# Performance work log

Hardware: AMD Instinct MI355X
Metric: run time of the kernel (lower is better)

Reference implementation:

```python
import jax, jax.numpy as jnp
import numpy as np

D_IN = 1024
D_OUT = 1024


def setup_inputs() -> dict:
    key = jax.random.key(0)
    kx, kq, kk, kv = jax.random.split(key, 4)
    x = jax.random.normal(kx, (4, 2048, D_IN), dtype=jnp.float32)
    s = 1.0 / np.sqrt(D_IN)
    Wq = jax.random.normal(kq, (D_IN, D_OUT), dtype=jnp.float32) * s
    Wk = jax.random.normal(kk, (D_IN, D_OUT), dtype=jnp.float32) * s
    Wv = jax.random.normal(kv, (D_IN, D_OUT), dtype=jnp.float32) * s
    return {"x": x, "Wq": Wq, "Wk": Wk, "Wv": Wv}


def reference(x, Wq, Wk, Wv):
    # x: [B, S, d_in]; W*: [d_in, d_out]
    B, S, _ = x.shape
    q = x @ Wq  # [B, S, d_out]
    k = x @ Wk
    v = x @ Wv
    scale = 1.0 / jnp.sqrt(jnp.asarray(k.shape[-1], x.dtype))
    scores = jnp.einsum("bqd,bkd->bqk", q, k) * scale  # [B, S, S]
    # causal mask: positions j > i masked to -inf (triu, diagonal=1)
    causal = jnp.tril(jnp.ones((S, S), dtype=bool))
    scores = jnp.where(causal[None, :, :], scores, -jnp.inf)
    attn = jax.nn.softmax(scores, axis=-1)  # dropout p=0.0 -> identity
    return jnp.einsum("bqk,bkd->bqd", attn, v)
```

## Files before the change

kernel.cpp:

```cpp
#include <hip/hip_runtime.h>
#include <hip/hip_bf16.h>

#define NB 4
#define SB 2048
#define DD 1024
#define BM 128
#define BN 128
#define BK 32

typedef __attribute__((ext_vector_type(8))) short bf16x8;
typedef __attribute__((ext_vector_type(4))) short bf16x4;
typedef __attribute__((ext_vector_type(4))) float f32x4;
typedef unsigned int u32;

__device__ __forceinline__ float bf2f(unsigned short u) {
    return __uint_as_float(((u32)u) << 16);
}
__device__ __forceinline__ short f2bf(float f) {
    u32 u = __float_as_uint(f);
    u32 r = (u + 0x7fffu + ((u >> 16) & 1u)) >> 16;
    return (short)r;
}

__device__ __forceinline__ void wait_vm8() {
    asm volatile("s_waitcnt vmcnt(8)" ::: "memory");
}
__device__ __forceinline__ void wait_vm6() {
    asm volatile("s_waitcnt vmcnt(6)" ::: "memory");
}
__device__ __forceinline__ void wait_vm0() {
    asm volatile("s_waitcnt vmcnt(0)" ::: "memory");
}
__device__ __forceinline__ void barrier_raw() {
    __builtin_amdgcn_s_barrier();
    asm volatile("" ::: "memory");
}

__device__ __forceinline__ void mfma_step(const short* As, const short* Bs,
                                          f32x4 (&acc)[4][4], int lane, int wave)
{
    const int wm = (wave >> 1) * 64, wn = (wave & 1) * 64;
    const int fr = lane & 15;
    const int quad = lane >> 4;
    bf16x8 af[4], bf[4];
#pragma unroll
    for (int t = 0; t < 4; t++) {
        af[t] = *(const bf16x8*)&As[(wm + t * 16 + fr) * BK + quad * 8];
        bf[t] = *(const bf16x8*)&Bs[(wn + t * 16 + fr) * BK + quad * 8];
    }
#pragma unroll
    for (int mt = 0; mt < 4; mt++)
#pragma unroll
        for (int nt = 0; nt < 4; nt++)
            acc[mt][nt] = __builtin_amdgcn_mfma_f32_16x16x32_bf16(
                af[mt], bf[nt], acc[mt][nt], 0, 0, 0);
}

__device__ __forceinline__ void mfma_step_pv_swz(const short* As,
                                                 const short* Bs,
                                                 f32x4 (&acc)[2][4], int lane,
                                                 int wave)
{
    const int wm = wave * 32;
    const int fr = lane & 15;
    const int qa = (lane >> 4) ^ ((fr >> 1) & 3);
    bf16x8 af[2], bf[4];
#pragma unroll
    for (int t = 0; t < 2; t++)
        af[t] = *(const bf16x8*)&As[(wm + t * 16 + fr) * BK + qa * 8];
#pragma unroll
    for (int t = 0; t < 4; t++)
        bf[t] = *(const bf16x8*)&Bs[(t * 16 + fr) * BK + qa * 8];
#pragma unroll
    for (int mt = 0; mt < 2; mt++)
#pragma unroll
        for (int nt = 0; nt < 4; nt++)
            acc[mt][nt] = __builtin_amdgcn_mfma_f32_16x16x32_bf16(
                af[mt], bf[nt], acc[mt][nt], 0, 0, 0);
}

__device__ __forceinline__ void mfma_step256_swz(const short* As,
                                                 const short* Bs,
                                                 f32x4 (&acc)[8][4], int lane,
                                                 int wave)
{
    const int wm = (wave >> 2) * 128;
    const int wn = (wave & 3) * 64;
    const int fr = lane & 15;
    const int qa = (lane >> 4) ^ ((fr >> 1) & 3);
    bf16x8 af[8], bf[4];
#pragma unroll
    for (int t = 0; t < 8; t++)
        af[t] = *(const bf16x8*)&As[(wm + t * 16 + fr) * BK + qa * 8];
#pragma unroll
    for (int t = 0; t < 4; t++)
        bf[t] = *(const bf16x8*)&Bs[(wn + t * 16 + fr) * BK + qa * 8];
#pragma unroll
    for (int mt = 0; mt < 8; mt++)
#pragma unroll
        for (int nt = 0; nt < 4; nt++)
            acc[mt][nt] = __builtin_amdgcn_mfma_f32_16x16x32_bf16(
                af[mt], bf[nt], acc[mt][nt], 0, 0, 0);
}

__device__ __forceinline__ void stage128x32(const short* __restrict__ g, int ld,
                                            short* lds, int tid) {
    const int wave = tid >> 6, lane = tid & 63;
    const int r = lane >> 2;
    const int c = ((lane & 3) ^ ((lane >> 3) & 3)) * 8;
#pragma unroll
    for (int i = 0; i < 2; i++) {
        const int chunk = wave * 2 + i;
        const short* gp = g + (size_t)(chunk * 16 + r) * ld + c;
        __builtin_amdgcn_global_load_lds(
            (const __attribute__((address_space(1))) u32*)gp,
            (__attribute__((address_space(3))) u32*)(lds + chunk * 512 + lane * 8),
            16, 0, 0);
    }
}

__device__ __forceinline__ void stage64x32(const short* __restrict__ g, int ld,
                                           short* lds, int tid) {
    const int wave = tid >> 6, lane = tid & 63;
    const int r = lane >> 2;
    const int c = ((lane & 3) ^ ((lane >> 3) & 3)) * 8;
    const short* gp = g + (size_t)(wave * 16 + r) * ld + c;
    __builtin_amdgcn_global_load_lds(
        (const __attribute__((address_space(1))) u32*)gp,
        (__attribute__((address_space(3))) u32*)(lds + wave * 512 + lane * 8),
        16, 0, 0);
}

__device__ __forceinline__ void stage256x64(const short* __restrict__ g, int ld,
                                            short* base, int tid) {
    const int w = tid >> 6, l = tid & 63;
    const int lr = l >> 2;
    const int lc = ((l & 3) ^ ((l >> 3) & 3)) * 8;
#pragma unroll
    for (int i = 0; i < 4; i++) {
        const int ks = i >> 1;
        const int row = (i & 1) * 128 + w * 16 + lr;
        const short* gp = g + (size_t)row * ld + ks * 32 + lc;
        __builtin_amdgcn_global_load_lds(
            (const __attribute__((address_space(1))) u32*)gp,
            (__attribute__((address_space(3))) u32*)(base + i * 4096 + w * 512 + l * 8),
            16, 0, 0);
    }
}

__device__ __forceinline__ void stage_f32_128x32(const float* __restrict__ g,
                                                 int ld, short* lds, int tid) {
    const int r = tid >> 1;
    const int c = (tid & 1) * 16;
    const float* gp = &g[(size_t)r * ld + c];
    float4 v0 = *(const float4*)(gp + 0);
    float4 v1 = *(const float4*)(gp + 4);
    float4 v2 = *(const float4*)(gp + 8);
    float4 v3 = *(const float4*)(gp + 12);
    bf16x8 o0, o1;
    o0[0] = f2bf(v0.x); o0[1] = f2bf(v0.y); o0[2] = f2bf(v0.z); o0[3] = f2bf(v0.w);
    o0[4] = f2bf(v1.x); o0[5] = f2bf(v1.y); o0[6] = f2bf(v1.z); o0[7] = f2bf(v1.w);
    o1[0] = f2bf(v2.x); o1[1] = f2bf(v2.y); o1[2] = f2bf(v2.z); o1[3] = f2bf(v2.w);
    o1[4] = f2bf(v3.x); o1[5] = f2bf(v3.y); o1[6] = f2bf(v3.z); o1[7] = f2bf(v3.w);
    *(bf16x8*)&lds[r * BK + c] = o0;
    *(bf16x8*)&lds[r * BK + c + 8] = o1;
}

__global__ __launch_bounds__(256) void prep_mm(
    const float* __restrict__ x, const float* __restrict__ Wq,
    const float* __restrict__ Wk, const float* __restrict__ Wv,
    short* __restrict__ xb, short* __restrict__ Wvt, float* __restrict__ Mp4)
{
    __shared__ short As[BM * BK], Bs[BN * BK];
    __shared__ short t[64][65];
    const int bx = blockIdx.x;
    const int tid = threadIdx.x;
    if (bx < 256) {
        const int ch = bx >> 6;
        const int t64 = bx & 63;
        const int m0 = (t64 >> 3) * BM;
        const int n0 = (t64 & 7) * BN;
        const int kbase = ch * 256;
        const int lane = tid & 63, wave = tid >> 6;
        f32x4 acc[4][4];
#pragma unroll
        for (int a = 0; a < 4; a++)
#pragma unroll
            for (int b = 0; b < 4; b++) acc[a][b] = (f32x4){0.f, 0.f, 0.f, 0.f};
        for (int k0 = 0; k0 < 256; k0 += BK) {
            stage_f32_128x32(Wk + (size_t)m0 * DD + kbase + k0, DD, As, tid);
            stage_f32_128x32(Wq + (size_t)n0 * DD + kbase + k0, DD, Bs, tid);
            __syncthreads();
            mfma_step(As, Bs, acc, lane, wave);
            __syncthreads();
        }
        const int wm = (wave >> 1) * 64, wn = (wave & 1) * 64;
        const int fr = lane & 15, quad = lane >> 4;
        float* Mc = Mp4 + (size_t)ch * DD * DD;
#pragma unroll
        for (int mt = 0; mt < 4; mt++)
#pragma unroll
            for (int nt = 0; nt < 4; nt++)
#pragma unroll
                for (int r = 0; r < 4; r++) {
                    const size_t m = m0 + wm + mt * 16 + quad * 4 + r;
                    const size_t n = n0 + wn + nt * 16 + fr;
                    Mc[m * DD + n] = acc[mt][nt][r];
                }
        return;
    }
    if (bx < 4352) {
        const size_t i = ((size_t)(bx - 256) * 256 + tid) * 8;
        float4 a = *(const float4*)&x[i];
        float4 b = *(const float4*)&x[i + 4];
        bf16x8 o;
        o[0] = f2bf(a.x); o[1] = f2bf(a.y); o[2] = f2bf(a.z); o[3] = f2bf(a.w);
        o[4] = f2bf(b.x); o[5] = f2bf(b.y); o[6] = f2bf(b.z); o[7] = f2bf(b.w);
        *(bf16x8*)&xb[i] = o;
        return;
    }
    const int rr = bx - 4352;
    const int k0 = (rr & 15) * 64;
    const int n0 = (rr >> 4) * 64;
    {
        const int r = tid >> 4;
        const int c = (tid & 15) * 4;
#pragma unroll
        for (int i = 0; i < 4; i++) {
            float4 v = *(const float4*)&Wv[(size_t)(k0 + i * 16 + r) * DD + n0 + c];
            t[i * 16 + r][c + 0] = f2bf(v.x);
            t[i * 16 + r][c + 1] = f2bf(v.y);
            t[i * 16 + r][c + 2] = f2bf(v.z);
            t[i * 16 + r][c + 3] = f2bf(v.w);
        }
    }
    __syncthreads();
    {
        const int r = tid >> 3;
        const int c = (tid & 7) * 8;
#pragma unroll
        for (int i = 0; i < 2; i++) {
            bf16x8 o;
#pragma unroll
            for (int j = 0; j < 8; j++) o[j] = t[c + j][i * 32 + r];
            *(bf16x8*)&Wvt[(size_t)(n0 + i * 32 + r) * DD + k0 + c] = o;
        }
    }
}

__global__ __launch_bounds__(256) void mm_reduce(const float* __restrict__ Mp4,
                                                 short* __restrict__ Mp)
{
    const size_t e = ((size_t)blockIdx.x * 256 + threadIdx.x) * 4;
    const size_t N = (size_t)DD * DD;
    float4 s = *(const float4*)&Mp4[e];
#pragma unroll
    for (int c = 1; c < 4; c++) {
        float4 p = *(const float4*)&Mp4[c * N + e];
        s.x += p.x; s.y += p.y; s.z += p.z; s.w += p.w;
    }
    bf16x4 o;
    o[0] = f2bf(s.x); o[1] = f2bf(s.y); o[2] = f2bf(s.z); o[3] = f2bf(s.w);
    *(bf16x4*)&Mp[e] = o;
}

__global__ __launch_bounds__(512) void tv_gemm(
    const short* __restrict__ xb, const short* __restrict__ Mp,
    const short* __restrict__ Wvt, short* __restrict__ T,
    short* __restrict__ Vt)
{
    __shared__ short lds[2 * 32768];
    const int lin = blockIdx.x + 4 * blockIdx.y;
    const int swz = (lin & 7) * 16 + (lin >> 3);
    const int n0 = (swz & 3) * 256;
    const int m0 = (swz >> 2) * 256;
    const int isv = blockIdx.z;
    const short* Bt = isv ? Wvt : Mp;
    const short* Ap = xb + (size_t)m0 * DD;
    const short* Bp = Bt + (size_t)n0 * DD;
    const int tid = threadIdx.x;
    const int lane = tid & 63, wave = tid >> 6;
    f32x4 acc[8][4];
#pragma unroll
    for (int a = 0; a < 8; a++)
#pragma unroll
        for (int b = 0; b < 4; b++) acc[a][b] = (f32x4){0.f, 0.f, 0.f, 0.f};

    stage256x64(Ap, DD, lds, tid);
    stage256x64(Bp, DD, lds + 16384, tid);
    for (int j = 0; j < 16; ++j) {
        const int cur = j & 1;
        short* slot = lds + cur * 32768;
        if (j < 15) {
            short* nxt = lds + (cur ^ 1) * 32768;
            stage256x64(Ap + (j + 1) * 64, DD, nxt, tid);
            stage256x64(Bp + (j + 1) * 64, DD, nxt + 16384, tid);
            wait_vm8();
        } else {
            wait_vm0();
        }
        barrier_raw();
        __builtin_amdgcn_s_setprio(1);
        mfma_step256_swz(slot, slot + 16384, acc, lane, wave);
        mfma_step256_swz(slot + 8192, slot + 16384 + 8192, acc, lane, wave);
        __builtin_amdgcn_s_setprio(0);
        barrier_raw();
    }

    const int wm = (wave >> 2) * 128, wn = (wave & 3) * 64;
    const int fr = lane & 15, quad = lane >> 4;
    if (!isv) {
#pragma unroll
        for (int mt = 0; mt < 8; mt++)
#pragma unroll
            for (int nt = 0; nt < 4; nt++)
#pragma unroll
                for (int r = 0; r < 4; r++) {
                    const size_t m = m0 + wm + mt * 16 + quad * 4 + r;
                    const size_t n = n0 + wn + nt * 16 + fr;
                    T[m * DD + n] = f2bf(acc[mt][nt][r]);
                }
    } else {
        const int bb = m0 >> 11;
        const int s0 = (m0 & (SB - 1)) + wm + quad * 4;
        short* Vb = Vt + (size_t)bb * DD * SB;
#pragma unroll
        for (int mt = 0; mt < 8; mt++)
#pragma unroll
            for (int nt = 0; nt < 4; nt++) {
                const size_t n = n0 + wn + nt * 16 + fr;
                const size_t s = s0 + mt * 16;
                bf16x4 o;
#pragma unroll
                for (int r = 0; r < 4; r++) o[r] = f2bf(acc[mt][nt][r]);
                *(bf16x4*)&Vb[n * SB + s] = o;
            }
    }
}

__global__ __launch_bounds__(256) void scores_mfma(
    const short* __restrict__ T, const short* __restrict__ xb,
    short* __restrict__ Sc)
{
    const int bx = blockIdx.x;
    const int idx = (bx & 7) * 34 + (bx >> 3);
    int qt = (int)((__fsqrt_rn(4.f * idx + 1.f) - 1.f) * 0.5f);
    while ((qt + 1) * (qt + 2) <= idx) qt++;
    while (qt * (qt + 1) > idx) qt--;
    const int kt = idx - qt * (qt + 1);
    const int qm0 = qt * BM;
    const int kn0 = kt * 64;
    const int b = blockIdx.y;
    __shared__ short As[2 * BM * BK], Bs[2 * 64 * BK];
    const short* Tq = T + (size_t)b * SB * DD + (size_t)qm0 * DD;
    const short* Xk = xb + (size_t)b * SB * DD + (size_t)kn0 * DD;
    short* Sb = Sc + (size_t)b * SB * SB;
    const int tid = threadIdx.x;
    const int lane = tid & 63, wave = tid >> 6;
    f32x4 acc[2][4];
#pragma unroll
    for (int a = 0; a < 2; a++)
#pragma unroll
        for (int c = 0; c < 4; c++) acc[a][c] = (f32x4){0.f, 0.f, 0.f, 0.f};
    for (int k0 = 0; k0 < DD; k0 += 2 * BK) {
        stage128x32(Tq + k0, DD, As, tid);
        stage128x32(Tq + k0 + BK, DD, As + BM * BK, tid);
        stage64x32(Xk + k0, DD, Bs, tid);
        stage64x32(Xk + k0 + BK, DD, Bs + 64 * BK, tid);
        __syncthreads();
        mfma_step_pv_swz(As, Bs, acc, lane, wave);
        mfma_step_pv_swz(As + BM * BK, Bs + 64 * BK, acc, lane, wave);
        __syncthreads();
    }
    const int fr = lane & 15, quad = lane >> 4;
    const float scale = 0.03125f;
#pragma unroll
    for (int mt = 0; mt < 2; mt++)
#pragma unroll
        for (int nt = 0; nt < 4; nt++)
#pragma unroll
            for (int r = 0; r < 4; r++) {
                const size_t q = qm0 + wave * 32 + mt * 16 + quad * 4 + r;
                const size_t k = kn0 + nt * 16 + fr;
                Sb[q * SB + k] = f2bf(acc[mt][nt][r] * scale);
            }
}

__global__ __launch_bounds__(256) void softmax_kernel(short* __restrict__ Sc)
{
    const int row = blockIdx.x;
    const int i = row & (SB - 1);
    const int jlim = ((i >> 7) + 1) << 7;
    short* r = Sc + (size_t)row * SB;
    const int t = threadIdx.x;
    const int lane = t & 63, wave = t >> 6;
    __shared__ float red[8];

    const int j0 = t * 8;
    bf16x8 in = {0, 0, 0, 0, 0, 0, 0, 0};
    if (j0 <= i) in = *(const bf16x8*)&r[j0];
    float v[8];
    float mx = -1e30f;
#pragma unroll
    for (int e = 0; e < 8; e++) {
        const float s = (j0 + e <= i) ? bf2f((unsigned short)in[e]) : -1e30f;
        v[e] = s;
        mx = fmaxf(mx, s);
    }
#pragma unroll
    for (int o = 32; o > 0; o >>= 1) mx = fmaxf(mx, __shfl_down(mx, o));
    if (lane == 0) red[wave] = mx;
    __syncthreads();
    mx = fmaxf(fmaxf(red[0], red[1]), fmaxf(red[2], red[3]));

    float sum = 0.f;
#pragma unroll
    for (int e = 0; e < 8; e++) {
        const float x = (j0 + e <= i) ? __expf(v[e] - mx) : 0.f;
        v[e] = x;
        sum += x;
    }
#pragma unroll
    for (int o = 32; o > 0; o >>= 1) sum += __shfl_down(sum, o);
    if (lane == 0) red[4 + wave] = sum;
    __syncthreads();
    const float inv = 1.0f / (red[4] + red[5] + red[6] + red[7]);
    if (j0 < jlim) {
        bf16x8 o;
#pragma unroll
        for (int e = 0; e < 8; e++) o[e] = f2bf(v[e] * inv);
        *(bf16x8*)&r[j0] = o;
    }
}

__global__ __launch_bounds__(256) void pv_mfma(
    const short* __restrict__ P, const short* __restrict__ Vt,
    float* __restrict__ O)
{
    __shared__ short As[4 * BM * BK];
    __shared__ short Bs[4 * 64 * BK];
    const int n0 = blockIdx.x * 64;
    const int pair = blockIdx.y;
    const int b = blockIdx.z;
    const short* Pb = P + (size_t)b * SB * SB;
    const short* Vb = Vt + (size_t)b * DD * SB;
    float* Ob = O + (size_t)b * SB * DD;
    const int tid = threadIdx.x;
    const int lane = tid & 63, wave = tid >> 6;
    const int fr = lane & 15, quad = lane >> 4;
    for (int half = 0; half < 2; ++half) {
        const int qt = half ? (15 - pair) : pair;
        const int qm0 = qt * BM;
        const int nj = (qt + 1) * 2;
        const short* Pq = Pb + (size_t)qm0 * SB;
        const short* Vn = Vb + (size_t)n0 * SB;
        f32x4 acc[2][4];
#pragma unroll
        for (int a = 0; a < 2; a++)
#pragma unroll
            for (int c = 0; c < 4; c++) acc[a][c] = (f32x4){0.f, 0.f, 0.f, 0.f};
        stage128x32(Pq, SB, As, tid);
        stage128x32(Pq + BK, SB, As + BM * BK, tid);
        stage64x32(Vn, SB, Bs, tid);
        stage64x32(Vn + BK, SB, Bs + 64 * BK, tid);
        for (int j = 0; j < nj; ++j) {
            const int cur = j & 1;
            const short* as = As + cur * (2 * BM * BK);
            const short* bs = Bs + cur * (2 * 64 * BK);
            if (j + 1 < nj) {
                const int off = (j + 1) * 64;
                short* an = As + (cur ^ 1) * (2 * BM * BK);
                short* bn = Bs + (cur ^ 1) * (2 * 64 * BK);
                stage128x32(Pq + off, SB, an, tid);
                stage128x32(Pq + off + BK, SB, an + BM * BK, tid);
                stage64x32(Vn + off, SB, bn, tid);
                stage64x32(Vn + off + BK, SB, bn + 64 * BK, tid);
                wait_vm6();
            } else {
                wait_vm0();
            }
            barrier_raw();
            mfma_step_pv_swz(as, bs, acc, lane, wave);
            mfma_step_pv_swz(as + BM * BK, bs + 64 * BK, acc, lane, wave);
            barrier_raw();
        }
#pragma unroll
        for (int mt = 0; mt < 2; mt++)
#pragma unroll
            for (int nt = 0; nt < 4; nt++)
#pragma unroll
                for (int r = 0; r < 4; r++) {
                    const size_t q = qm0 + wave * 32 + mt * 16 + quad * 4 + r;
                    const size_t n = n0 + nt * 16 + fr;
                    Ob[q * DD + n] = acc[mt][nt][r];
                }
    }
}

extern "C" void kernel_launch(void* const* d_in, const int* in_sizes, int n_in,
                              void* d_out, int out_size, void* d_ws, size_t ws_size,
                              hipStream_t stream)
{
    const float* x  = (const float*)d_in[0];
    const float* Wq = (const float*)d_in[1];
    const float* Wk = (const float*)d_in[2];
    const float* Wv = (const float*)d_in[3];
    float* out = (float*)d_out;

    const size_t XE = (size_t)NB * SB * DD;
    const size_t WE = (size_t)DD * DD;
    short* xb  = (short*)d_ws;
    short* T   = xb + XE;
    short* Vt  = T + XE;
    short* Sc  = Vt + XE;
    float* Pp  = (float*)(Sc + (size_t)NB * SB * SB);
    short* Wvt = (short*)(Pp + (size_t)NB * 1024 * DD);
    short* Mp  = Wvt + WE;
    float* Mp4 = (float*)Sc;

    prep_mm<<<dim3(256 + 4096 + 256), 256, 0, stream>>>(
        x, Wq, Wk, Wv, xb, Wvt, Mp4);
    mm_reduce<<<dim3(1024), 256, 0, stream>>>(Mp4, Mp);
    tv_gemm<<<dim3(4, 32, 2), 512, 0, stream>>>(xb, Mp, Wvt, T, Vt);
    scores_mfma<<<dim3(272, NB), 256, 0, stream>>>(T, xb, Sc);
    softmax_kernel<<<dim3(NB * SB), 256, 0, stream>>>(Sc);
    pv_mfma<<<dim3(DD / 64, 8, NB), 256, 0, stream>>>(Sc, Vt, out);
}
```

Baseline: 222.6 us.

## Widen PV kernel tiles to 128x128 with swizzled MFMA fragment loads

The PV GEMM now computes a 128x128 output tile per block instead of 128x64, and each wave owns a 64x64 sub-tile using a new swizzled MFMA step. The grid shrinks from 512 to 256 blocks, and the wait count is adjusted for the extra V staging loads. It also raises wave priority around the MFMA section. The goal is better reuse of the staged P tile and fewer P reloads, at the cost of fewer blocks for the GPU's many CUs and more LDS and registers per block.

```diff
diff --git a/kernel.cpp b/kernel.cpp
--- a/kernel.cpp
+++ b/kernel.cpp
@@ -25,9 +25,6 @@
 __device__ __forceinline__ void wait_vm8() {
     asm volatile("s_waitcnt vmcnt(8)" ::: "memory");
 }
-__device__ __forceinline__ void wait_vm6() {
-    asm volatile("s_waitcnt vmcnt(6)" ::: "memory");
-}
 __device__ __forceinline__ void wait_vm0() {
     asm volatile("s_waitcnt vmcnt(0)" ::: "memory");
 }
@@ -47,6 +44,27 @@
     for (int t = 0; t < 4; t++) {
         af[t] = *(const bf16x8*)&As[(wm + t * 16 + fr) * BK + quad * 8];
         bf[t] = *(const bf16x8*)&Bs[(wn + t * 16 + fr) * BK + quad * 8];
+    }
+#pragma unroll
+    for (int mt = 0; mt < 4; mt++)
+#pragma unroll
+        for (int nt = 0; nt < 4; nt++)
+            acc[mt][nt] = __builtin_amdgcn_mfma_f32_16x16x32_bf16(
+                af[mt], bf[nt], acc[mt][nt], 0, 0, 0);
+}
+
+__device__ __forceinline__ void mfma_step_swz(const short* As, const short* Bs,
+                                              f32x4 (&acc)[4][4], int lane,
+                                              int wave)
+{
+    const int wm = (wave >> 1) * 64, wn = (wave & 1) * 64;
+    const int fr = lane & 15;
+    const int qa = (lane >> 4) ^ ((fr >> 1) & 3);
+    bf16x8 af[4], bf[4];
+#pragma unroll
+    for (int t = 0; t < 4; t++) {
+        af[t] = *(const bf16x8*)&As[(wm + t * 16 + fr) * BK + qa * 8];
+        bf[t] = *(const bf16x8*)&Bs[(wn + t * 16 + fr) * BK + qa * 8];
     }
 #pragma unroll
     for (int mt = 0; mt < 4; mt++)
@@ -437,10 +455,9 @@
     const short* __restrict__ P, const short* __restrict__ Vt,
     float* __restrict__ O)
 {
-    __shared__ short As[4 * BM * BK];
-    __shared__ short Bs[4 * 64 * BK];
-    const int n0 = blockIdx.x * 64;
-    const int pair = blockIdx.y;
+    __shared__ short As[2 * 8192], Bs[2 * 8192];
+    const int pair = blockIdx.x;
+    const int n0 = blockIdx.y * 128;
     const int b = blockIdx.z;
     const short* Pb = P + (size_t)b * SB * SB;
     const short* Vb = Vt + (size_t)b * DD * SB;
@@ -454,44 +471,47 @@
         const int nj = (qt + 1) * 2;
         const short* Pq = Pb + (size_t)qm0 * SB;
         const short* Vn = Vb + (size_t)n0 * SB;
-        f32x4 acc[2][4];
-#pragma unroll
-        for (int a = 0; a < 2; a++)
+        f32x4 acc[4][4];
+#pragma unroll
+        for (int a = 0; a < 4; a++)
 #pragma unroll
             for (int c = 0; c < 4; c++) acc[a][c] = (f32x4){0.f, 0.f, 0.f, 0.f};
         stage128x32(Pq, SB, As, tid);
-        stage128x32(Pq + BK, SB, As + BM * BK, tid);
-        stage64x32(Vn, SB, Bs, tid);
-        stage64x32(Vn + BK, SB, Bs + 64 * BK, tid);
+        stage128x32(Pq + BK, SB, As + 4096, tid);
+        stage128x32(Vn, SB, Bs, tid);
+        stage128x32(Vn + BK, SB, Bs + 4096, tid);
         for (int j = 0; j < nj; ++j) {
             const int cur = j & 1;
-            const short* as = As + cur * (2 * BM * BK);
-            const short* bs = Bs + cur * (2 * 64 * BK);
+            const short* as = As + cur * 8192;
+            const short* bs = Bs + cur * 8192;
             if (j + 1 < nj) {
                 const int off = (j + 1) * 64;
-                short* an = As + (cur ^ 1) * (2 * BM * BK);
-                short* bn = Bs + (cur ^ 1) * (2 * 64 * BK);
+                short* an = As + (cur ^ 1) * 8192;
+                short* bn = Bs + (cur ^ 1) * 8192;
                 stage128x32(Pq + off, SB, an, tid);
-                stage128x32(Pq + off + BK, SB, an + BM * BK, tid);
-                stage64x32(Vn + off, SB, bn, tid);
-                stage64x32(Vn + off + BK, SB, bn + 64 * BK, tid);
-                wait_vm6();
+                stage128x32(Pq + off + BK, SB, an + 4096, tid);
+                stage128x32(Vn + off, SB, bn, tid);
+                stage128x32(Vn + off + BK, SB, bn + 4096, tid);
+                wait_vm8();
             } else {
                 wait_vm0();
             }
             barrier_raw();
-            mfma_step_pv_swz(as, bs, acc, lane, wave);
-            mfma_step_pv_swz(as + BM * BK, bs + 64 * BK, acc, lane, wave);
+            __builtin_amdgcn_s_setprio(1);
+            mfma_step_swz(as, bs, acc, lane, wave);
+            mfma_step_swz(as + 4096, bs + 4096, acc, lane, wave);
+            __builtin_amdgcn_s_setprio(0);
             barrier_raw();
         }
-#pragma unroll
-        for (int mt = 0; mt < 2; mt++)
+        const int wm = (wave >> 1) * 64, wn = (wave & 1) * 64;
+#pragma unroll
+        for (int mt = 0; mt < 4; mt++)
 #pragma unroll
             for (int nt = 0; nt < 4; nt++)
 #pragma unroll
                 for (int r = 0; r < 4; r++) {
-                    const size_t q = qm0 + wave * 32 + mt * 16 + quad * 4 + r;
-                    const size_t n = n0 + nt * 16 + fr;
+                    const size_t q = qm0 + wm + mt * 16 + quad * 4 + r;
+                    const size_t n = n0 + wn + nt * 16 + fr;
                     Ob[q * DD + n] = acc[mt][nt][r];
                 }
     }
@@ -524,5 +544,5 @@
     tv_gemm<<<dim3(4, 32, 2), 512, 0, stream>>>(xb, Mp, Wvt, T, Vt);
     scores_mfma<<<dim3(272, NB), 256, 0, stream>>>(T, xb, Sc);
     softmax_kernel<<<dim3(NB * SB), 256, 0, stream>>>(Sc);
-    pv_mfma<<<dim3(DD / 64, 8, NB), 256, 0, stream>>>(Sc, Vt, out);
-}
+    pv_mfma<<<dim3(8, 8, NB), 256, 0, stream>>>(Sc, Vt, out);
+}
```

Result: slower. 227.9 us (median of 2 runs) (+2.4%).
